# Kernel optimization log

Measured on AMD Instinct MI355X. Metric: run time of the kernel, lower is better.

## Reference

```python
import jax, jax.numpy as jnp
import numpy as np

N, F_IN, H, C1, CH, NCLS, E = 10000, 512, 8, 30, 64, 64, 160000


def gat_conv(x, src, dst, W, a_src, a_dst, b):
    # x: [N, Fin]; W: [Fin, H*C]; a_src/a_dst: [H, C]; b: [H*C]
    n, = (x.shape[0],)
    C = a_src.shape[1]
    h = (x @ W).reshape(n, H, C)                        # [N,H,C]
    asrc = jnp.einsum('nhc,hc->nh', h, a_src)           # [N,H]
    adst = jnp.einsum('nhc,hc->nh', h, a_dst)           # [N,H]
    alpha = jax.nn.leaky_relu(asrc[src] + adst[dst], 0.2)  # [E,H]
    # segment softmax over incoming edges of each destination node
    m = jax.ops.segment_max(alpha, dst, num_segments=n)
    m = jax.lax.stop_gradient(jnp.where(jnp.isfinite(m), m, 0.0))
    e = jnp.exp(alpha - m[dst])
    s = jax.ops.segment_sum(e, dst, num_segments=n)
    w = e / (s[dst] + 1e-16)                            # [E,H]
    out = jax.ops.segment_sum(w[:, :, None] * h[src], dst, num_segments=n)
    return out.reshape(n, H * C) + b


def setup_inputs() -> dict:
    key = jax.random.key(0)
    ks = jax.random.split(key, 12)
    x = jax.random.normal(ks[0], (N, F_IN), dtype=jnp.float32)
    edge_index = jax.random.randint(ks[1], (2, E), 0, N, dtype=jnp.int64)
    sc = lambda fin: 1.0 / np.sqrt(fin)
    return {
        'x': x,
        'edge_index': edge_index,
        'W1': jax.random.normal(ks[2], (F_IN, H * C1), jnp.float32) * sc(F_IN),
        'a1_src': jax.random.normal(ks[3], (H, C1), jnp.float32) * sc(C1),
        'a1_dst': jax.random.normal(ks[4], (H, C1), jnp.float32) * sc(C1),
        'b1': jnp.zeros((H * C1,), jnp.float32),
        'W2': jax.random.normal(ks[5], (H * C1, H * CH), jnp.float32) * sc(H * C1),
        'a2_src': jax.random.normal(ks[6], (H, CH), jnp.float32) * sc(CH),
        'a2_dst': jax.random.normal(ks[7], (H, CH), jnp.float32) * sc(CH),
        'b2': jnp.zeros((H * CH,), jnp.float32),
        'Wlin': jax.random.normal(ks[8], (H * CH, NCLS), jnp.float32) * sc(H * CH),
        'blin': jnp.zeros((NCLS,), jnp.float32),
    }


def reference(x, edge_index, W1, a1_src, a1_dst, b1, W2, a2_src, a2_dst, b2, Wlin, blin):
    n = x.shape[0]
    loops = jnp.arange(n, dtype=edge_index.dtype)
    src = jnp.concatenate([edge_index[0], loops])
    dst = jnp.concatenate([edge_index[1], loops])
    # dropout is identity in eval mode
    h1 = jax.nn.elu(gat_conv(x, src, dst, W1, a1_src, a1_dst, b1))
    h = gat_conv(h1, src, dst, W2, a2_src, a2_dst, b2)
    out = h @ Wlin + blin
    return (out, h)
```

## Files before the change

kernel.cpp:

```cpp
#include <hip/hip_runtime.h>
#include <type_traits>

typedef unsigned short ushort_t;
typedef float v4f __attribute__((ext_vector_type(4)));
typedef short v8s __attribute__((ext_vector_type(8)));
typedef unsigned short u16x8 __attribute__((ext_vector_type(8)));
typedef unsigned short u16x4v __attribute__((ext_vector_type(4)));

#define NN    10000
#define EE    160000
#define FIN   512
#define NH    8
#define C1    30
#define HC1   240
#define HC1P  256
#define C2    64
#define HC2   512
#define NCLS  64

#define TS1 (HC1P * FIN)
#define TS2 (HC2 * HC1P)
#define TS3 (NCLS * HC2)


__global__ __launch_bounds__(1024) void scan_kernel(const int* __restrict__ counts,
                                                    int* __restrict__ row_start, int n) {
    __shared__ int sums[1024];
    int t = threadIdx.x;
    const int chunk = (n + 1023) / 1024;
    int beg = t * chunk;
    int end = min(beg + chunk, n);
    int s = 0;
    for (int i = beg; i < end; ++i) s += counts[i];
    sums[t] = s;
    __syncthreads();
    for (int off = 1; off < 1024; off <<= 1) {
        int v = (t >= off) ? sums[t - off] : 0;
        __syncthreads();
        sums[t] += v;
        __syncthreads();
    }
    int run = (t == 0) ? 0 : sums[t - 1];
    for (int i = beg; i < end; ++i) {
        row_start[i] = run;
        run += counts[i];
    }
    if (t == 1023) row_start[n] = sums[1023];
}

__global__ __launch_bounds__(256) void scatter_kernel(const int* __restrict__ src,
                                                      const int* __restrict__ dst,
                                                      const int* __restrict__ row_start,
                                                      int* __restrict__ cursor,
                                                      int* __restrict__ edge_src, int E) {
    int e = blockIdx.x * blockDim.x + threadIdx.x;
    if (e < E) {
        int d = dst[e];
        int pos = row_start[d] + atomicAdd(&cursor[d], 1);
        edge_src[pos] = src[e];
    }
}


__device__ __forceinline__ void split1(float v, ushort_t& h, ushort_t& l) {
    unsigned u = __float_as_uint(v);
    unsigned rh = u + 0x7FFFu + ((u >> 16) & 1u);
    h = (ushort_t)(rh >> 16);
    float hf = __uint_as_float((unsigned)h << 16);
    float rem = v - hf;
    unsigned u2 = __float_as_uint(rem);
    unsigned rl = u2 + 0x7FFFu + ((u2 >> 16) & 1u);
    l = (ushort_t)(rl >> 16);
}

__device__ __forceinline__ ushort_t f2bf(float v) {
    unsigned u = __float_as_uint(v);
    return (ushort_t)((u + 0x7FFFu + ((u >> 16) & 1u)) >> 16);
}

__device__ __forceinline__ float bf2f(ushort_t u) {
    return __uint_as_float((unsigned)u << 16);
}


__global__ __launch_bounds__(256) void prep_kernel(
    const float* __restrict__ W1, const float* __restrict__ W2,
    const float* __restrict__ Wl,
    const float* __restrict__ a1s, const float* __restrict__ a1d,
    const int* __restrict__ dst,
    ushort_t* __restrict__ t1h, ushort_t* __restrict__ t1l,
    ushort_t* __restrict__ t2h, ushort_t* __restrict__ t2l,
    ushort_t* __restrict__ t3h, ushort_t* __restrict__ t3l,
    float* __restrict__ a1sP, float* __restrict__ a1dP,
    int* __restrict__ counts) {
    int idx = blockIdx.x * 256 + threadIdx.x;
    if (idx < TS1) {
        int n = idx >> 9, k = idx & 511;
        int cc = n & 31;
        float v = (cc < 30) ? W1[(size_t)k * HC1 + ((n >> 5) * 30 + cc)] : 0.f;
        ushort_t h, l;
        split1(v, h, l);
        t1h[idx] = h;
        t1l[idx] = l;
    } else if (idx < TS1 + TS2) {
        int lo = idx - TS1;
        int n = lo >> 8, k = lo & 255;
        int cc = k & 31;
        float v = (cc < 30) ? W2[(size_t)((k >> 5) * 30 + cc) * HC2 + n] : 0.f;
        ushort_t h, l;
        split1(v, h, l);
        t2h[lo] = h;
        t2l[lo] = l;
    } else if (idx < TS1 + TS2 + TS3) {
        int lo = idx - TS1 - TS2;
        int n = lo >> 9, k = lo & 511;
        float v = Wl[(size_t)k * NCLS + n];
        ushort_t h, l;
        split1(v, h, l);
        t3h[lo] = h;
        t3l[lo] = l;
    } else if (idx < TS1 + TS2 + TS3 + 2 * HC1P) {
        int j = idx - (TS1 + TS2 + TS3);
        int c = j & (HC1P - 1);
        int cc = c & 31;
        float vs = (cc < 30) ? a1s[(c >> 5) * 30 + cc] : 0.f;
        float vd = (cc < 30) ? a1d[(c >> 5) * 30 + cc] : 0.f;
        if (j < HC1P) a1sP[c] = vs;
        else          a1dP[c] = vd;
    } else {
        int e = idx - (TS1 + TS2 + TS3 + 2 * HC1P);
        if (e < EE) atomicAdd(&counts[dst[e]], 1);
    }
}


template <int TM, int TN, bool ASPLIT, bool BIAS, bool WF32, bool WBF, int TPH>
__global__ __launch_bounds__(256) void gemm_mfma(const float* __restrict__ A,
                                                 const ushort_t* __restrict__ Ath,
                                                 const ushort_t* __restrict__ Atl,
                                                 const ushort_t* __restrict__ Bth,
                                                 const ushort_t* __restrict__ Btl,
                                                 const float* __restrict__ bias,
                                                 float* __restrict__ C,
                                                 ushort_t* __restrict__ Cbf,
                                                 const float* __restrict__ att_s,
                                                 const float* __restrict__ att_d,
                                                 float* __restrict__ asrc,
                                                 float* __restrict__ adst,
                                                 int M, int K, int CS) {
    constexpr int ROWS = 32 * TM;
    constexpr int BN = 32 * TN;
    constexpr int SK = 40;
    __shared__ ushort_t Ah[ROWS * SK], Al[ROWS * SK];
    __shared__ ushort_t Bh[BN * SK], Bl[BN * SK];
    const int t    = threadIdx.x;
    const int lane = t & 63;
    const int wave = t >> 6;
    const int quad = lane >> 4;
    const int l16  = lane & 15;
    const int wm   = wave >> 1;
    const int wn   = wave & 1;
    const int bm   = blockIdx.x * ROWS;
    const int bn   = blockIdx.y * BN;

    v4f acc[TM][TN];
    #pragma unroll
    for (int i = 0; i < TM; ++i)
        #pragma unroll
        for (int j = 0; j < TN; ++j) acc[i][j] = 0.f;

    for (int k0 = 0; k0 < K; k0 += 32) {
        if (k0) __syncthreads();
        #pragma unroll
        for (int idx = t; idx < ROWS * 4; idx += 256) {
            int row = idx >> 2;
            int kcb = (idx & 3) * 8;
            int gm = bm + row;
            u16x8 hv, lv;
            if (ASPLIT) {
                if (gm < M) {
                    size_t go = (size_t)gm * K + k0 + kcb;
                    hv = *(const u16x8*)(Ath + go);
                    lv = *(const u16x8*)(Atl + go);
                } else {
                    #pragma unroll
                    for (int i = 0; i < 8; ++i) { hv[i] = 0; lv[i] = 0; }
                }
            } else {
                float va[8];
                if (gm < M) {
                    const float* Ap = A + (size_t)gm * K + k0 + kcb;
                    float4 p = *(const float4*)Ap;
                    float4 q = *(const float4*)(Ap + 4);
                    va[0] = p.x; va[1] = p.y; va[2] = p.z; va[3] = p.w;
                    va[4] = q.x; va[5] = q.y; va[6] = q.z; va[7] = q.w;
                } else {
                    #pragma unroll
                    for (int i = 0; i < 8; ++i) va[i] = 0.f;
                }
                #pragma unroll
                for (int i = 0; i < 8; ++i) {
                    ushort_t h, l;
                    split1(va[i], h, l);
                    hv[i] = h;
                    lv[i] = l;
                }
            }
            *(u16x8*)&Ah[row * SK + kcb] = hv;
            *(u16x8*)&Al[row * SK + kcb] = lv;
        }
        #pragma unroll
        for (int idx = t; idx < BN * 4; idx += 256) {
            int row = idx >> 2;
            int kcb = (idx & 3) * 8;
            size_t go = (size_t)(bn + row) * K + k0 + kcb;
            *(u16x8*)&Bh[row * SK + kcb] = *(const u16x8*)(Bth + go);
            *(u16x8*)&Bl[row * SK + kcb] = *(const u16x8*)(Btl + go);
        }
        __syncthreads();

        v8s ah[TM], al2[TM], bh2[TN], bl2[TN];
        #pragma unroll
        for (int tt = 0; tt < TM; ++tt) {
            int ma = (wm * 16 * TM + tt * 16 + l16) * SK + quad * 8;
            ah[tt]  = *(const v8s*)&Ah[ma];
            al2[tt] = *(const v8s*)&Al[ma];
        }
        #pragma unroll
        for (int tn = 0; tn < TN; ++tn) {
            int nb = (wn * 16 * TN + tn * 16 + l16) * SK + quad * 8;
            bh2[tn] = *(const v8s*)&Bh[nb];
            bl2[tn] = *(const v8s*)&Bl[nb];
        }
        #pragma unroll
        for (int tm = 0; tm < TM; ++tm)
            #pragma unroll
            for (int tn = 0; tn < TN; ++tn) {
                acc[tm][tn] = __builtin_amdgcn_mfma_f32_16x16x32_bf16(
                    ah[tm], bh2[tn], acc[tm][tn], 0, 0, 0);
                acc[tm][tn] = __builtin_amdgcn_mfma_f32_16x16x32_bf16(
                    ah[tm], bl2[tn], acc[tm][tn], 0, 0, 0);
                acc[tm][tn] = __builtin_amdgcn_mfma_f32_16x16x32_bf16(
                    al2[tm], bh2[tn], acc[tm][tn], 0, 0, 0);
            }
    }

    #pragma unroll
    for (int tm = 0; tm < TM; ++tm) {
        #pragma unroll
        for (int tn = 0; tn < TN; ++tn) {
            int row0 = bm + wm * 16 * TM + tm * 16 + quad * 4;
            int col  = bn + wn * 16 * TN + tn * 16 + l16;
            float badd = BIAS ? bias[col] : 0.f;
            #pragma unroll
            for (int reg = 0; reg < 4; ++reg) {
                int row = row0 + reg;
                if (row < M) {
                    float v = acc[tm][tn][reg] + badd;
                    if (WF32) C[(size_t)row * CS + col] = v;
                    if (WBF) Cbf[(size_t)row * CS + col] = f2bf(v);
                }
            }
        }
    }

    if constexpr (TPH > 0) {
        constexpr int GR = TN / TPH;
        float aS[TN], aD[TN];
        #pragma unroll
        for (int tn = 0; tn < TN; ++tn) {
            int col = bn + wn * 16 * TN + tn * 16 + l16;
            aS[tn] = att_s[col];
            aD[tn] = att_d[col];
        }
        #pragma unroll
        for (int tm = 0; tm < TM; ++tm) {
            #pragma unroll
            for (int reg = 0; reg < 4; ++reg) {
                #pragma unroll
                for (int g = 0; g < GR; ++g) {
                    float ss = 0.f, sd = 0.f;
                    #pragma unroll
                    for (int ti = 0; ti < TPH; ++ti) {
                        int tn = g * TPH + ti;
                        ss += acc[tm][tn][reg] * aS[tn];
                        sd += acc[tm][tn][reg] * aD[tn];
                    }
                    #pragma unroll
                    for (int off = 1; off < 16; off <<= 1) {
                        ss += __shfl_xor(ss, off);
                        sd += __shfl_xor(sd, off);
                    }
                    if (l16 == 0) {
                        int row = bm + wm * 16 * TM + tm * 16 + quad * 4 + reg;
                        if (row < M) {
                            int head = (bn + wn * 16 * TN + g * 16 * TPH) / (16 * TPH);
                            asrc[row * NH + head] = ss;
                            adst[row * NH + head] = sd;
                        }
                    }
                }
            }
        }
    }
}


template <int CPL, bool ELU, bool OSPLIT, bool PADB>
__global__ __launch_bounds__(256) void agg_u(const ushort_t* __restrict__ hb,
                                             const float* __restrict__ asrc,
                                             const float* __restrict__ adst,
                                             const int* __restrict__ row_start,
                                             const int* __restrict__ edge_src,
                                             const float* __restrict__ bias,
                                             float* __restrict__ outf,
                                             ushort_t* __restrict__ outh,
                                             ushort_t* __restrict__ outl,
                                             int n) {
    constexpr int RSB = CPL * 64;
    using VT = typename std::conditional<CPL == 8, u16x8, u16x4v>::type;
    const int d    = (blockIdx.x * blockDim.x + threadIdx.x) >> 6;
    const int lane = threadIdx.x & 63;
    if (d >= n) return;
    const int head = lane >> 3;

    const float adh = (lane < NH) ? adst[d * NH + lane] : 0.f;

    float m, s;
    float ac[CPL];
    {
        float a = (lane < NH) ? asrc[d * NH + lane] + adh : 0.f;
        a = fmaxf(a, 0.2f * a);
        m = a;
        s = 1.f;
        VT u = *(const VT*)(hb + (size_t)d * RSB + CPL * lane);
        #pragma unroll
        for (int i = 0; i < CPL; ++i) ac[i] = bf2f(u[i]);
    }

    const int beg = row_start[d];
    const int end = row_start[d + 1];

    auto LD = [&](int eb, VT* rr, float* ss) {
        int i0 = edge_src[eb], i1 = edge_src[eb + 1];
        int i2 = edge_src[eb + 2], i3 = edge_src[eb + 3];
        rr[0] = *(const VT*)(hb + (size_t)i0 * RSB + CPL * lane);
        rr[1] = *(const VT*)(hb + (size_t)i1 * RSB + CPL * lane);
        rr[2] = *(const VT*)(hb + (size_t)i2 * RSB + CPL * lane);
        rr[3] = *(const VT*)(hb + (size_t)i3 * RSB + CPL * lane);
        if (lane < NH) {
            ss[0] = asrc[i0 * NH + lane];
            ss[1] = asrc[i1 * NH + lane];
            ss[2] = asrc[i2 * NH + lane];
            ss[3] = asrc[i3 * NH + lane];
        } else {
            ss[0] = ss[1] = ss[2] = ss[3] = 0.f;
        }
    };
    auto PR = [&](const VT* rr, const float* ss) {
        float a0 = ss[0] + adh, a1 = ss[1] + adh, a2 = ss[2] + adh, a3 = ss[3] + adh;
        a0 = fmaxf(a0, 0.2f * a0);
        a1 = fmaxf(a1, 0.2f * a1);
        a2 = fmaxf(a2, 0.2f * a2);
        a3 = fmaxf(a3, 0.2f * a3);
        float mn = fmaxf(m, fmaxf(fmaxf(a0, a1), fmaxf(a2, a3)));
        float al = __expf(m - mn);
        float w0 = __expf(a0 - mn);
        float w1 = __expf(a1 - mn);
        float w2 = __expf(a2 - mn);
        float w3 = __expf(a3 - mn);
        s = s * al + (w0 + w1) + (w2 + w3);
        m = mn;
        float alc = __shfl(al, head);
        float c0 = __shfl(w0, head);
        float c1 = __shfl(w1, head);
        float c2 = __shfl(w2, head);
        float c3 = __shfl(w3, head);
        #pragma unroll
        for (int i = 0; i < CPL; ++i)
            ac[i] = ac[i] * alc + c0 * bf2f(rr[0][i]) + c1 * bf2f(rr[1][i]) +
                    c2 * bf2f(rr[2][i]) + c3 * bf2f(rr[3][i]);
    };

    int e = beg;
    const int ng = (end - beg) >> 2;
    if (ng > 0) {
        VT cr[4];
        float cs[4];
        LD(e, cr, cs);
        for (int g = 1; g < ng; ++g) {
            VT nr[4];
            float ns[4];
            LD(e + 4 * g, nr, ns);
            PR(cr, cs);
            #pragma unroll
            for (int j = 0; j < 4; ++j) { cr[j] = nr[j]; cs[j] = ns[j]; }
        }
        PR(cr, cs);
        e += 4 * ng;
    }
    for (; e < end; ++e) {
        int i0 = edge_src[e];
        VT r0 = *(const VT*)(hb + (size_t)i0 * RSB + CPL * lane);
        float a0 = (lane < NH) ? asrc[i0 * NH + lane] + adh : 0.f;
        a0 = fmaxf(a0, 0.2f * a0);
        float mn = fmaxf(m, a0);
        float al = __expf(m - mn);
        float w0 = __expf(a0 - mn);
        s = s * al + w0;
        m = mn;
        float alc = __shfl(al, head);
        float c0w = __shfl(w0, head);
        #pragma unroll
        for (int i = 0; i < CPL; ++i) ac[i] = ac[i] * alc + c0w * bf2f(r0[i]);
    }

    float inv = 1.f / s;
    float ivc = __shfl(inv, head);
    float o[CPL];
    if constexpr (PADB) {
        const int c = CPL * lane;
        const int cc = c & 31;
        const int bbase = (c >> 5) * 30 + cc;
        #pragma unroll
        for (int i = 0; i < CPL; ++i) {
            float b = (cc + i < 30) ? bias[bbase + i] : 0.f;
            o[i] = ac[i] * ivc + b;
        }
    } else {
        #pragma unroll
        for (int i = 0; i < CPL; ++i) o[i] = ac[i] * ivc + bias[CPL * lane + i];
    }
    if (ELU) {
        #pragma unroll
        for (int i = 0; i < CPL; ++i) o[i] = (o[i] > 0.f) ? o[i] : __expf(o[i]) - 1.f;
    }
    if constexpr (OSPLIT) {
        VT hh, ll;
        #pragma unroll
        for (int i = 0; i < CPL; ++i) {
            ushort_t h2, l2;
            split1(o[i], h2, l2);
            hh[i] = h2;
            ll[i] = l2;
        }
        *(VT*)(outh + (size_t)d * RSB + CPL * lane) = hh;
        *(VT*)(outl + (size_t)d * RSB + CPL * lane) = ll;
    } else {
        float4* orow = (float4*)(outf + (size_t)d * RSB);
        #pragma unroll
        for (int q = 0; q < CPL / 4; ++q) {
            float4 v;
            v.x = o[4 * q + 0];
            v.y = o[4 * q + 1];
            v.z = o[4 * q + 2];
            v.w = o[4 * q + 3];
            orow[(CPL / 4) * lane + q] = v;
        }
    }
}


extern "C" void kernel_launch(void* const* d_in, const int* in_sizes, int n_in,
                              void* d_out, int out_size, void* d_ws, size_t ws_size,
                              hipStream_t stream) {
    const float* x      = (const float*)d_in[0];
    const int*   eidx   = (const int*)d_in[1];
    const float* W1     = (const float*)d_in[2];
    const float* a1_src = (const float*)d_in[3];
    const float* a1_dst = (const float*)d_in[4];
    const float* b1     = (const float*)d_in[5];
    const float* W2     = (const float*)d_in[6];
    const float* a2_src = (const float*)d_in[7];
    const float* a2_dst = (const float*)d_in[8];
    const float* b2     = (const float*)d_in[9];
    const float* Wlin   = (const float*)d_in[10];
    const float* blin   = (const float*)d_in[11];

    const int* src = eidx;
    const int* dst = eidx + EE;

    float* out0  = (float*)d_out;
    float* h_out = (float*)d_out + (size_t)NN * NCLS;

    float* f = (float*)d_ws;
    float* asrc1 = f;
    float* adst1 = asrc1 + NN * NH;
    float* asrc2 = adst1 + NN * NH;
    float* adst2 = asrc2 + NN * NH;
    float* a1sP  = adst2 + NN * NH;
    float* a1dP  = a1sP + HC1P;
    ushort_t* w1t_h = (ushort_t*)(a1dP + HC1P);
    ushort_t* w1t_l = w1t_h + TS1;
    ushort_t* w2t_h = w1t_l + TS1;
    ushort_t* w2t_l = w2t_h + TS2;
    ushort_t* wlt_h = w2t_l + TS2;
    ushort_t* wlt_l = wlt_h + TS3;
    ushort_t* h1p_bf = wlt_l + TS3;
    ushort_t* h1h    = h1p_bf + (size_t)NN * HC1P;
    ushort_t* h1l    = h1h + (size_t)NN * HC1P;
    ushort_t* h2p_bf = h1l + (size_t)NN * HC1P;
    int* counts    = (int*)(h2p_bf + (size_t)NN * HC2);
    int* cursor    = counts + NN;
    int* row_start = cursor + NN;
    int* edge_src  = row_start + NN + 1;

    hipMemsetAsync(counts, 0, 2 * NN * sizeof(int), stream);

    {
        const int total = TS1 + TS2 + TS3 + 2 * HC1P + EE;
        prep_kernel<<<(total + 255) / 256, 256, 0, stream>>>(
            W1, W2, Wlin, a1_src, a1_dst, dst, w1t_h, w1t_l, w2t_h, w2t_l,
            wlt_h, wlt_l, a1sP, a1dP, counts);
    }
    scan_kernel<<<1, 1024, 0, stream>>>(counts, row_start, NN);
    scatter_kernel<<<(EE + 255) / 256, 256, 0, stream>>>(src, dst, row_start, cursor,
                                                         edge_src, EE);

    const int MB = (NN + 63) / 64;

    {
        dim3 grid(MB, HC1P / 128);
        gemm_mfma<2, 4, false, false, false, true, 2><<<grid, 256, 0, stream>>>(
            x, nullptr, nullptr, w1t_h, w1t_l, nullptr, nullptr, h1p_bf,
            a1sP, a1dP, asrc1, adst1, NN, FIN, HC1P);
    }
    agg_u<4, true, true, true><<<(NN + 3) / 4, 256, 0, stream>>>(
        h1p_bf, asrc1, adst1, row_start, edge_src, b1, nullptr, h1h, h1l, NN);

    {
        dim3 grid(MB, HC2 / 128);
        gemm_mfma<2, 4, true, false, false, true, 4><<<grid, 256, 0, stream>>>(
            nullptr, h1h, h1l, w2t_h, w2t_l, nullptr, nullptr, h2p_bf,
            a2_src, a2_dst, asrc2, adst2, NN, HC1P, HC2);
    }
    agg_u<8, false, false, false><<<(NN + 3) / 4, 256, 0, stream>>>(
        h2p_bf, asrc2, adst2, row_start, edge_src, b2, h_out, nullptr, nullptr, NN);

    {
        dim3 grid((NN + 31) / 32, NCLS / 64);
        gemm_mfma<1, 2, false, true, true, false, 0><<<grid, 256, 0, stream>>>(
            h_out, nullptr, nullptr, wlt_h, wlt_l, blin, out0, nullptr,
            nullptr, nullptr, nullptr, nullptr, NN, HC2, NCLS);
    }
}
```

Measured before the change: 230.8 us.

## Double-buffer GEMM tiles with async global-to-LDS loads and pre-split all A operands

The GEMM kernel now stages A and B tiles into a swizzled, double-buffered LDS region using global_load_lds 16-byte copies. The next k-slice is fetched while the current one feeds MFMA, and the per-row bounds checks are dropped by padding the A buffers to NP rows. The input x and the layer-2 output are now split into bf16 hi/lo pairs ahead of time (in prep and in the agg epilogue), so every GEMM reads pre-split bf16 instead of converting fp32 inside the loop. This costs an extra pass over x and extra workspace traffic. The scatter cursor is also seeded from the scan, which removes one memset range and a row_start read.

After: 223.6 us. 3.1% less time.

```diff
diff --git a/kernel.cpp b/kernel.cpp
--- a/kernel.cpp
+++ b/kernel.cpp
@@ -8,6 +8,7 @@
 typedef unsigned short u16x4v __attribute__((ext_vector_type(4)));
 
 #define NN    10000
+#define NP    10048
 #define EE    160000
 #define FIN   512
 #define NH    8
@@ -21,10 +22,20 @@
 #define TS1 (HC1P * FIN)
 #define TS2 (HC2 * HC1P)
 #define TS3 (NCLS * HC2)
+#define XS  (NN * FIN / 4)
+
+#define GLOBAL_AS __attribute__((address_space(1)))
+#define LDS_AS    __attribute__((address_space(3)))
+
+__device__ __forceinline__ void async_cp16(const void* g, void* l) {
+    __builtin_amdgcn_global_load_lds((const GLOBAL_AS unsigned int*)g,
+                                     (LDS_AS unsigned int*)l, 16, 0, 0);
+}
 
 
 __global__ __launch_bounds__(1024) void scan_kernel(const int* __restrict__ counts,
-                                                    int* __restrict__ row_start, int n) {
+                                                    int* __restrict__ row_start,
+                                                    int* __restrict__ cursor, int n) {
     __shared__ int sums[1024];
     int t = threadIdx.x;
     const int chunk = (n + 1023) / 1024;
@@ -43,6 +54,7 @@
     int run = (t == 0) ? 0 : sums[t - 1];
     for (int i = beg; i < end; ++i) {
         row_start[i] = run;
+        cursor[i] = run;
         run += counts[i];
     }
     if (t == 1023) row_start[n] = sums[1023];
@@ -50,13 +62,12 @@
 
 __global__ __launch_bounds__(256) void scatter_kernel(const int* __restrict__ src,
                                                       const int* __restrict__ dst,
-                                                      const int* __restrict__ row_start,
                                                       int* __restrict__ cursor,
                                                       int* __restrict__ edge_src, int E) {
     int e = blockIdx.x * blockDim.x + threadIdx.x;
     if (e < E) {
         int d = dst[e];
-        int pos = row_start[d] + atomicAdd(&cursor[d], 1);
+        int pos = atomicAdd(&cursor[d], 1);
         edge_src[pos] = src[e];
     }
 }
@@ -84,16 +95,32 @@
 
 
 __global__ __launch_bounds__(256) void prep_kernel(
+    const float* __restrict__ x,
     const float* __restrict__ W1, const float* __restrict__ W2,
     const float* __restrict__ Wl,
     const float* __restrict__ a1s, const float* __restrict__ a1d,
     const int* __restrict__ dst,
+    ushort_t* __restrict__ xh, ushort_t* __restrict__ xl,
     ushort_t* __restrict__ t1h, ushort_t* __restrict__ t1l,
     ushort_t* __restrict__ t2h, ushort_t* __restrict__ t2l,
     ushort_t* __restrict__ t3h, ushort_t* __restrict__ t3l,
     float* __restrict__ a1sP, float* __restrict__ a1dP,
     int* __restrict__ counts) {
     int idx = blockIdx.x * 256 + threadIdx.x;
+    if (idx < XS) {
+        int i = idx << 2;
+        float4 v = *(const float4*)(x + i);
+        ushort_t h, l;
+        u16x4v hh, ll;
+        split1(v.x, h, l); hh[0] = h; ll[0] = l;
+        split1(v.y, h, l); hh[1] = h; ll[1] = l;
+        split1(v.z, h, l); hh[2] = h; ll[2] = l;
+        split1(v.w, h, l); hh[3] = h; ll[3] = l;
+        *(u16x4v*)(xh + i) = hh;
+        *(u16x4v*)(xl + i) = ll;
+        return;
+    }
+    idx -= XS;
     if (idx < TS1) {
         int n = idx >> 9, k = idx & 511;
         int cc = n & 31;
@@ -134,9 +161,8 @@
 }
 
 
-template <int TM, int TN, bool ASPLIT, bool BIAS, bool WF32, bool WBF, int TPH>
-__global__ __launch_bounds__(256) void gemm_mfma(const float* __restrict__ A,
-                                                 const ushort_t* __restrict__ Ath,
+template <int TM, int TN, bool BIAS, bool WF32, bool WBF, int TPH>
+__global__ __launch_bounds__(256) void gemm_mfma(const ushort_t* __restrict__ Ath,
                                                  const ushort_t* __restrict__ Atl,
                                                  const ushort_t* __restrict__ Bth,
                                                  const ushort_t* __restrict__ Btl,
@@ -149,10 +175,18 @@
                                                  float* __restrict__ adst,
                                                  int M, int K, int CS) {
     constexpr int ROWS = 32 * TM;
-    constexpr int BN = 32 * TN;
-    constexpr int SK = 40;
-    __shared__ ushort_t Ah[ROWS * SK], Al[ROWS * SK];
-    __shared__ ushort_t Bh[BN * SK], Bl[BN * SK];
+    constexpr int BN   = 32 * TN;
+    constexpr int CA = ROWS / 16;
+    constexpr int CB = BN / 16;
+    constexpr int TOT = 2 * (CA + CB);
+    static_assert(TOT % 4 == 0, "chunks must split across 4 waves");
+    constexpr int PW = TOT / 4;
+    constexpr int AOFF_L = ROWS * 32;
+    constexpr int BOFF_H = ROWS * 64;
+    constexpr int BOFF_L = ROWS * 64 + BN * 32;
+    constexpr int BUFSZ  = (ROWS + BN) * 64;
+    __shared__ ushort_t lds[2][BUFSZ];
+
     const int t    = threadIdx.x;
     const int lane = t & 63;
     const int wave = t >> 6;
@@ -163,74 +197,66 @@
     const int bm   = blockIdx.x * ROWS;
     const int bn   = blockIdx.y * BN;
 
+    const ushort_t* gsrc[PW];
+    int ldst[PW];
+    {
+        const int rr = lane >> 2;
+        const int q  = lane & 3;
+        const int sw = (q ^ (rr & 3)) << 3;
+        #pragma unroll
+        for (int c = 0; c < PW; ++c) {
+            int j = wave * PW + c;
+            const ushort_t* gt;
+            int off, jj, gb;
+            if (j < CA)               { gt = Ath; jj = j;              off = 0;      gb = bm; }
+            else if (j < 2 * CA)      { gt = Atl; jj = j - CA;         off = AOFF_L; gb = bm; }
+            else if (j < 2 * CA + CB) { gt = Bth; jj = j - 2 * CA;     off = BOFF_H; gb = bn; }
+            else                      { gt = Btl; jj = j - 2 * CA - CB; off = BOFF_L; gb = bn; }
+            gsrc[c] = gt + (size_t)(gb + jj * 16 + rr) * K + sw;
+            ldst[c] = off + jj * 512;
+        }
+    }
+
+    int aoff[TM], boff[TN];
+    #pragma unroll
+    for (int tt = 0; tt < TM; ++tt) {
+        int r = wm * 16 * TM + tt * 16 + l16;
+        aoff[tt] = r * 32 + ((quad ^ (r & 3)) << 3);
+    }
+    #pragma unroll
+    for (int tn = 0; tn < TN; ++tn) {
+        int r = wn * 16 * TN + tn * 16 + l16;
+        boff[tn] = r * 32 + ((quad ^ (r & 3)) << 3);
+    }
+
     v4f acc[TM][TN];
     #pragma unroll
     for (int i = 0; i < TM; ++i)
         #pragma unroll
         for (int j = 0; j < TN; ++j) acc[i][j] = 0.f;
 
+    #pragma unroll
+    for (int c = 0; c < PW; ++c) async_cp16(gsrc[c], &lds[0][ldst[c]]);
+
+    int cur = 0;
     for (int k0 = 0; k0 < K; k0 += 32) {
-        if (k0) __syncthreads();
-        #pragma unroll
-        for (int idx = t; idx < ROWS * 4; idx += 256) {
-            int row = idx >> 2;
-            int kcb = (idx & 3) * 8;
-            int gm = bm + row;
-            u16x8 hv, lv;
-            if (ASPLIT) {
-                if (gm < M) {
-                    size_t go = (size_t)gm * K + k0 + kcb;
-                    hv = *(const u16x8*)(Ath + go);
-                    lv = *(const u16x8*)(Atl + go);
-                } else {
-                    #pragma unroll
-                    for (int i = 0; i < 8; ++i) { hv[i] = 0; lv[i] = 0; }
-                }
-            } else {
-                float va[8];
-                if (gm < M) {
-                    const float* Ap = A + (size_t)gm * K + k0 + kcb;
-                    float4 p = *(const float4*)Ap;
-                    float4 q = *(const float4*)(Ap + 4);
-                    va[0] = p.x; va[1] = p.y; va[2] = p.z; va[3] = p.w;
-                    va[4] = q.x; va[5] = q.y; va[6] = q.z; va[7] = q.w;
-                } else {
-                    #pragma unroll
-                    for (int i = 0; i < 8; ++i) va[i] = 0.f;
-                }
-                #pragma unroll
-                for (int i = 0; i < 8; ++i) {
-                    ushort_t h, l;
-                    split1(va[i], h, l);
-                    hv[i] = h;
-                    lv[i] = l;
-                }
-            }
-            *(u16x8*)&Ah[row * SK + kcb] = hv;
-            *(u16x8*)&Al[row * SK + kcb] = lv;
-        }
-        #pragma unroll
-        for (int idx = t; idx < BN * 4; idx += 256) {
-            int row = idx >> 2;
-            int kcb = (idx & 3) * 8;
-            size_t go = (size_t)(bn + row) * K + k0 + kcb;
-            *(u16x8*)&Bh[row * SK + kcb] = *(const u16x8*)(Bth + go);
-            *(u16x8*)&Bl[row * SK + kcb] = *(const u16x8*)(Btl + go);
-        }
         __syncthreads();
-
+        if (k0 + 32 < K) {
+            #pragma unroll
+            for (int c = 0; c < PW; ++c)
+                async_cp16(gsrc[c] + k0 + 32, &lds[cur ^ 1][ldst[c]]);
+        }
+        const ushort_t* bufc = lds[cur];
         v8s ah[TM], al2[TM], bh2[TN], bl2[TN];
         #pragma unroll
         for (int tt = 0; tt < TM; ++tt) {
-            int ma = (wm * 16 * TM + tt * 16 + l16) * SK + quad * 8;
-            ah[tt]  = *(const v8s*)&Ah[ma];
-            al2[tt] = *(const v8s*)&Al[ma];
+            ah[tt]  = *(const v8s*)&bufc[aoff[tt]];
+            al2[tt] = *(const v8s*)&bufc[AOFF_L + aoff[tt]];
         }
         #pragma unroll
         for (int tn = 0; tn < TN; ++tn) {
-            int nb = (wn * 16 * TN + tn * 16 + l16) * SK + quad * 8;
-            bh2[tn] = *(const v8s*)&Bh[nb];
-            bl2[tn] = *(const v8s*)&Bl[nb];
+            bh2[tn] = *(const v8s*)&bufc[BOFF_H + boff[tn]];
+            bl2[tn] = *(const v8s*)&bufc[BOFF_L + boff[tn]];
         }
         #pragma unroll
         for (int tm = 0; tm < TM; ++tm)
@@ -243,6 +269,7 @@
                 acc[tm][tn] = __builtin_amdgcn_mfma_f32_16x16x32_bf16(
                     al2[tm], bh2[tn], acc[tm][tn], 0, 0, 0);
             }
+        cur ^= 1;
     }
 
     #pragma unroll
@@ -306,7 +333,7 @@
 }
 
 
-template <int CPL, bool ELU, bool OSPLIT, bool PADB>
+template <int CPL, bool ELU, bool OSPLIT, bool OF32, bool PADB>
 __global__ __launch_bounds__(256) void agg_u(const ushort_t* __restrict__ hb,
                                              const float* __restrict__ asrc,
                                              const float* __restrict__ adst,
@@ -446,7 +473,8 @@
         }
         *(VT*)(outh + (size_t)d * RSB + CPL * lane) = hh;
         *(VT*)(outl + (size_t)d * RSB + CPL * lane) = ll;
-    } else {
+    }
+    if constexpr (OF32) {
         float4* orow = (float4*)(outf + (size_t)d * RSB);
         #pragma unroll
         for (int q = 0; q < CPL / 4; ++q) {
@@ -490,7 +518,9 @@
     float* adst2 = asrc2 + NN * NH;
     float* a1sP  = adst2 + NN * NH;
     float* a1dP  = a1sP + HC1P;
-    ushort_t* w1t_h = (ushort_t*)(a1dP + HC1P);
+    ushort_t* xh    = (ushort_t*)(a1dP + HC1P);
+    ushort_t* xl    = xh + (size_t)NP * FIN;
+    ushort_t* w1t_h = xl + (size_t)NP * FIN;
     ushort_t* w1t_l = w1t_h + TS1;
     ushort_t* w2t_h = w1t_l + TS1;
     ushort_t* w2t_l = w2t_h + TS2;
@@ -498,49 +528,51 @@
     ushort_t* wlt_l = wlt_h + TS3;
     ushort_t* h1p_bf = wlt_l + TS3;
     ushort_t* h1h    = h1p_bf + (size_t)NN * HC1P;
-    ushort_t* h1l    = h1h + (size_t)NN * HC1P;
-    ushort_t* h2p_bf = h1l + (size_t)NN * HC1P;
-    int* counts    = (int*)(h2p_bf + (size_t)NN * HC2);
+    ushort_t* h1l    = h1h + (size_t)NP * HC1P;
+    ushort_t* h2p_bf = h1l + (size_t)NP * HC1P;
+    ushort_t* h2h    = h2p_bf + (size_t)NN * HC2;
+    ushort_t* h2l    = h2h + (size_t)NP * HC2;
+    int* counts    = (int*)(h2l + (size_t)NP * HC2);
     int* cursor    = counts + NN;
     int* row_start = cursor + NN;
     int* edge_src  = row_start + NN + 1;
 
-    hipMemsetAsync(counts, 0, 2 * NN * sizeof(int), stream);
+    hipMemsetAsync(counts, 0, NN * sizeof(int), stream);
 
     {
-        const int total = TS1 + TS2 + TS3 + 2 * HC1P + EE;
+        const int total = XS + TS1 + TS2 + TS3 + 2 * HC1P + EE;
         prep_kernel<<<(total + 255) / 256, 256, 0, stream>>>(
-            W1, W2, Wlin, a1_src, a1_dst, dst, w1t_h, w1t_l, w2t_h, w2t_l,
-            wlt_h, wlt_l, a1sP, a1dP, counts);
-    }
-    scan_kernel<<<1, 1024, 0, stream>>>(counts, row_start, NN);
-    scatter_kernel<<<(EE + 255) / 256, 256, 0, stream>>>(src, dst, row_start, cursor,
+            x, W1, W2, Wlin, a1_src, a1_dst, dst, xh, xl, w1t_h, w1t_l,
+            w2t_h, w2t_l, wlt_h, wlt_l, a1sP, a1dP, counts);
+    }
+    scan_kernel<<<1, 1024, 0, stream>>>(counts, row_start, cursor, NN);
+    scatter_kernel<<<(EE + 255) / 256, 256, 0, stream>>>(src, dst, cursor,
                                                          edge_src, EE);
 
     const int MB = (NN + 63) / 64;
 
     {
         dim3 grid(MB, HC1P / 128);
-        gemm_mfma<2, 4, false, false, false, true, 2><<<grid, 256, 0, stream>>>(
-            x, nullptr, nullptr, w1t_h, w1t_l, nullptr, nullptr, h1p_bf,
+        gemm_mfma<2, 4, false, false, true, 2><<<grid, 256, 0, stream>>>(
+            xh, xl, w1t_h, w1t_l, nullptr, nullptr, h1p_bf,
             a1sP, a1dP, asrc1, adst1, NN, FIN, HC1P);
     }
-    agg_u<4, true, true, true><<<(NN + 3) / 4, 256, 0, stream>>>(
+    agg_u<4, true, true, false, true><<<(NN + 3) / 4, 256, 0, stream>>>(
         h1p_bf, asrc1, adst1, row_start, edge_src, b1, nullptr, h1h, h1l, NN);
 
     {
         dim3 grid(MB, HC2 / 128);
-        gemm_mfma<2, 4, true, false, false, true, 4><<<grid, 256, 0, stream>>>(
-            nullptr, h1h, h1l, w2t_h, w2t_l, nullptr, nullptr, h2p_bf,
+        gemm_mfma<2, 4, false, false, true, 4><<<grid, 256, 0, stream>>>(
+            h1h, h1l, w2t_h, w2t_l, nullptr, nullptr, h2p_bf,
             a2_src, a2_dst, asrc2, adst2, NN, HC1P, HC2);
     }
-    agg_u<8, false, false, false><<<(NN + 3) / 4, 256, 0, stream>>>(
-        h2p_bf, asrc2, adst2, row_start, edge_src, b2, h_out, nullptr, nullptr, NN);
+    agg_u<8, false, true, true, false><<<(NN + 3) / 4, 256, 0, stream>>>(
+        h2p_bf, asrc2, adst2, row_start, edge_src, b2, h_out, h2h, h2l, NN);
 
     {
         dim3 grid((NN + 31) / 32, NCLS / 64);
-        gemm_mfma<1, 2, false, true, true, false, 0><<<grid, 256, 0, stream>>>(
-            h_out, nullptr, nullptr, wlt_h, wlt_l, blin, out0, nullptr,
+        gemm_mfma<1, 2, true, true, false, 0><<<grid, 256, 0, stream>>>(
+            h2h, h2l, wlt_h, wlt_l, blin, out0, nullptr,
             nullptr, nullptr, nullptr, nullptr, NN, HC2, NCLS);
     }
 }
```
